# Performance work log

Hardware: AMD Instinct MI355X
Metric: run time of the kernel (lower is better)

The kernel has to match this reference:

```python
import jax, jax.numpy as jnp
import numpy as np

MIN_POS = 1e-6
EPS = 1e-20
B, S, F_IN, E, H = 2, 1024, 768, 768, 12
DH = E // H   # nnmf in_features per head (64)
FH = E // H   # nnmf out_features per head (hidden_features=embed_dim default)
N_NNMF_ITERS = 3
N_ALPHA_ITERS = 3


def l1norm(x, axis=-1):
    # F.normalize(x, p=1, dim=axis, eps=1e-20) for non-negative x
    return x / jnp.maximum(jnp.sum(jnp.abs(x), axis=axis, keepdims=True), EPS)


def setup_inputs() -> dict:
    key = jax.random.key(0)
    k = jax.random.split(key, 6)
    return {
        "x": jax.random.normal(k[0], (B, S, F_IN), jnp.float32),
        "embed_w": jax.random.normal(k[1], (E, F_IN), jnp.float32) * 0.02,
        "embed_b": jnp.zeros((E,), jnp.float32),
        "nnmf_w": jax.random.uniform(k[2], (FH, DH), jnp.float32),  # non-negative NMF dictionary
        "out_w": jax.random.normal(k[3], (F_IN, E), jnp.float32) * 0.02,
        "out_b": jnp.zeros((F_IN,), jnp.float32),
    }


def reference(x, embed_w, embed_b, nnmf_w, out_w, out_b):
    # normalize NMF weight rows (p=1 over in_features), as nnmf_layer.normalize_weights
    W = nnmf_w / jnp.maximum(jnp.sum(nnmf_w, axis=1, keepdims=True), EPS)  # [FH, DH]

    # embed + clamp positive, split heads
    xe = jnp.clip(x @ embed_w.T + embed_b, MIN_POS)            # [B,S,E]
    xe = xe.reshape(B, S, H, DH)                                # [B,S,H,DH]

    # NNMFDense: prepared_input = l1-normalized input (normalize_input_dim=-1)
    inp = l1norm(xe)                                            # [B,S,H,DH]
    h = l1norm(jnp.ones((B, S, H, FH), x.dtype))                # init hidden
    rec = inp
    for _ in range(N_NNMF_ITERS):
        rec = l1norm(jnp.clip(h @ W, MIN_POS))                  # reconstruction [B,S,H,DH]
        h = l1norm(jnp.clip(h * ((inp / rec) @ W.T), MIN_POS))  # multiplicative update

    # normalize_h (p=1, dim=-1)
    h = l1norm(h)                                               # [B,S,H,FH] -> 'bohf'

    # alpha dynamics fixed point
    alpha = jnp.ones((B, H, S, S), x.dtype)                     # 'bhoi'
    h_rec_input = rec * inp                                     # [B,S,H,DH]
    for _ in range(N_ALPHA_ITERS):
        h_mixed = jnp.einsum('bohf,bhoi->bihf', h, alpha)       # [B,S,H,FH]
        arec_inv = 1.0 / (h_mixed @ W + EPS)                    # _reconstruct -> [B,S,H,DH]
        alpha = alpha * jnp.einsum('bohf,bihf->bhoi', h_rec_input, arec_inv)

    out = jnp.einsum('bohf,bhoi->bihf', h, alpha)               # [B,S,H,FH]
    out = out.reshape(B, S, E)                                  # flatten heads
    return out @ out_w.T + out_b                                # out_project
```

## Files before the change

### kernel.cpp

```cpp
#include <hip/hip_runtime.h>

#define B_  2
#define S_  1024
#define FIN 768
#define E_  768
#define H_  12
#define DH  64

typedef unsigned int uint;
typedef unsigned short ushort;
typedef __attribute__((ext_vector_type(8))) short short8;
typedef __attribute__((ext_vector_type(4))) float floatx4;

__device__ __forceinline__ float bcast_lane(float v, int l) {
    return __uint_as_float((uint)__builtin_amdgcn_readlane((int)__float_as_uint(v), l));
}

__device__ __forceinline__ void wsum64x2(float& a, float& b) {
#pragma unroll
    for (int m = 1; m < 64; m <<= 1) {
        a += __shfl_xor(a, m, 64);
        b += __shfl_xor(b, m, 64);
    }
}

__device__ __forceinline__ ushort f2bf(float f) {
    uint u = __float_as_uint(f);
    return (ushort)((u + 0x7fffu + ((u >> 16) & 1u)) >> 16);
}

__device__ __forceinline__ uint4 pack8(const ushort* p) {
    uint4 r;
    r.x = (uint)p[0] | ((uint)p[1] << 16);
    r.y = (uint)p[2] | ((uint)p[3] << 16);
    r.z = (uint)p[4] | ((uint)p[5] << 16);
    r.w = (uint)p[6] | ((uint)p[7] << 16);
    return r;
}

__global__ __launch_bounds__(256) void k_wprep(const float* __restrict__ nw,
                                               float* __restrict__ Wn,
                                               float* __restrict__ WnT,
                                               float* __restrict__ r1inv,
                                               float* __restrict__ zbase) {
    const int tid = threadIdx.x;
    if (blockIdx.x == 0) {
        __shared__ float Wl[64 * 65];
        const int f = tid >> 2, q = tid & 3;
        float v[16];
        float s = 0.f;
#pragma unroll
        for (int i = 0; i < 16; ++i) { v[i] = nw[f * 64 + q * 16 + i]; s += v[i]; }
        s += __shfl_xor(s, 1, 64);
        s += __shfl_xor(s, 2, 64);
        const float inv = 1.f / fmaxf(s, 1e-20f);
#pragma unroll
        for (int i = 0; i < 16; ++i) {
            float w = v[i] * inv;
            Wn[f * 64 + q * 16 + i] = w;
            WnT[(q * 16 + i) * 64 + f] = w;
            Wl[f * 65 + q * 16 + i] = w;
        }
        __syncthreads();
        if (tid < 64) {
            float cs = 0.f;
            for (int ff = 0; ff < 64; ++ff) cs += Wl[ff * 65 + tid];
            float t = fmaxf(cs * (1.f / 64.f), 1e-6f);
            float S = t;
#pragma unroll
            for (int m = 1; m < 64; m <<= 1) S += __shfl_xor(S, m, 64);
            S = fmaxf(S, 1e-20f);
            r1inv[tid] = S / t;
        }
    } else {
        const int i = (blockIdx.x - 1) * 1024 + tid * 4;
        if (i < 26112) {
            float4 z = make_float4(0.f, 0.f, 0.f, 0.f);
            *(float4*)(zbase + i) = z;
        }
    }
}

__global__ __launch_bounds__(256) void k_embed(const float* __restrict__ xs,
                                               const float* __restrict__ ew,
                                               const float* __restrict__ eb,
                                               float* __restrict__ inp) {
    __shared__ ushort As_hi[64 * 72], As_lo[64 * 72];
    __shared__ ushort Bs_hi[64 * 72], Bs_lo[64 * 72];
    __shared__ float RS[2][64];
    const int tid = threadIdx.x;
    const int head = blockIdx.y;
    const int tok0 = blockIdx.x * 64;
    const int wv = tid >> 6, lane = tid & 63;
    const int mbase = (wv >> 1) * 32, nbase = (wv & 1) * 32;
    const int lm = lane & 15, lq = lane >> 4;

    floatx4 acc[2][2];
#pragma unroll
    for (int si = 0; si < 2; ++si)
#pragma unroll
        for (int ti = 0; ti < 2; ++ti) acc[si][ti] = (floatx4)0.f;

    const int row = tid >> 2;
    const int kq = (tid & 3) * 16;
    const float* xrow = xs + (size_t)(tok0 + row) * FIN + kq;
    const float* wrow = ew + (size_t)(head * 64 + row) * FIN + kq;

    float4 pa[4], pb[4];
#pragma unroll
    for (int c = 0; c < 4; ++c) {
        pa[c] = *(const float4*)(xrow + c * 4);
        pb[c] = *(const float4*)(wrow + c * 4);
    }

    for (int kb = 0; kb < FIN; kb += 64) {
        __syncthreads();
        {
            ushort ah[16], al[16], bh[16], bl[16];
#pragma unroll
            for (int c4 = 0; c4 < 4; ++c4) {
                float va[4] = {pa[c4].x, pa[c4].y, pa[c4].z, pa[c4].w};
                float vb[4] = {pb[c4].x, pb[c4].y, pb[c4].z, pb[c4].w};
#pragma unroll
                for (int j = 0; j < 4; ++j) {
                    ushort h = f2bf(va[j]);
                    ah[c4 * 4 + j] = h;
                    al[c4 * 4 + j] = f2bf(va[j] - __uint_as_float(((uint)h) << 16));
                    ushort g = f2bf(vb[j]);
                    bh[c4 * 4 + j] = g;
                    bl[c4 * 4 + j] = f2bf(vb[j] - __uint_as_float(((uint)g) << 16));
                }
            }
            const int off = row * 72 + kq;
            *(uint4*)&As_hi[off]     = pack8(ah);
            *(uint4*)&As_hi[off + 8] = pack8(ah + 8);
            *(uint4*)&As_lo[off]     = pack8(al);
            *(uint4*)&As_lo[off + 8] = pack8(al + 8);
            *(uint4*)&Bs_hi[off]     = pack8(bh);
            *(uint4*)&Bs_hi[off + 8] = pack8(bh + 8);
            *(uint4*)&Bs_lo[off]     = pack8(bl);
            *(uint4*)&Bs_lo[off + 8] = pack8(bl + 8);
        }
        __syncthreads();
        if (kb + 64 < FIN) {
#pragma unroll
            for (int c = 0; c < 4; ++c) {
                pa[c] = *(const float4*)(xrow + kb + 64 + c * 4);
                pb[c] = *(const float4*)(wrow + kb + 64 + c * 4);
            }
        }
#pragma unroll
        for (int ch = 0; ch < 2; ++ch) {
            const int ko = ch * 32 + lq * 8;
            short8 ah[2], al[2], bh[2], bl[2];
#pragma unroll
            for (int si = 0; si < 2; ++si) {
                ah[si] = *(const short8*)&As_hi[(mbase + si * 16 + lm) * 72 + ko];
                al[si] = *(const short8*)&As_lo[(mbase + si * 16 + lm) * 72 + ko];
            }
#pragma unroll
            for (int ti = 0; ti < 2; ++ti) {
                bh[ti] = *(const short8*)&Bs_hi[(nbase + ti * 16 + lm) * 72 + ko];
                bl[ti] = *(const short8*)&Bs_lo[(nbase + ti * 16 + lm) * 72 + ko];
            }
#pragma unroll
            for (int si = 0; si < 2; ++si)
#pragma unroll
                for (int ti = 0; ti < 2; ++ti) {
                    acc[si][ti] = __builtin_amdgcn_mfma_f32_16x16x32_bf16(
                        ah[si], bh[ti], acc[si][ti], 0, 0, 0);
                    acc[si][ti] = __builtin_amdgcn_mfma_f32_16x16x32_bf16(
                        al[si], bh[ti], acc[si][ti], 0, 0, 0);
                    acc[si][ti] = __builtin_amdgcn_mfma_f32_16x16x32_bf16(
                        ah[si], bl[ti], acc[si][ti], 0, 0, 0);
                }
        }
    }

    const int half = wv & 1;
    const float b0 = eb[head * 64 + nbase + lm];
    const float b1 = eb[head * 64 + nbase + 16 + lm];
    float xe[2][2][4];
#pragma unroll
    for (int si = 0; si < 2; ++si) {
        float rs[4];
#pragma unroll
        for (int r = 0; r < 4; ++r) {
            float e0 = fmaxf(acc[si][0][r] + b0, 1e-6f);
            float e1 = fmaxf(acc[si][1][r] + b1, 1e-6f);
            xe[si][0][r] = e0; xe[si][1][r] = e1;
            rs[r] = e0 + e1;
        }
#pragma unroll
        for (int r = 0; r < 4; ++r) {
            rs[r] += __shfl_xor(rs[r], 1, 64);
            rs[r] += __shfl_xor(rs[r], 2, 64);
            rs[r] += __shfl_xor(rs[r], 4, 64);
            rs[r] += __shfl_xor(rs[r], 8, 64);
        }
        if (lm == 0) {
#pragma unroll
            for (int r = 0; r < 4; ++r)
                RS[half][mbase + si * 16 + lq * 4 + r] = rs[r];
        }
    }
    __syncthreads();
    const size_t obase = ((size_t)((tok0 >> 10) * 12 + head) * 1024 + (tok0 & 1023));
#pragma unroll
    for (int si = 0; si < 2; ++si)
#pragma unroll
        for (int r = 0; r < 4; ++r) {
            const int m = mbase + si * 16 + lq * 4 + r;
            const float inv = 1.f / fmaxf(RS[0][m] + RS[1][m], 1e-20f);
            float* op = inp + (obase + m) * 64;
            op[nbase + lm]      = xe[si][0][r] * inv;
            op[nbase + 16 + lm] = xe[si][1][r] * inv;
        }
}

__global__ __launch_bounds__(256) void k_nnmf(const float* __restrict__ inp,
                                              const float* __restrict__ Wn,
                                              const float* __restrict__ WnT,
                                              const float* __restrict__ r1inv,
                                              float* __restrict__ hout,
                                              float* __restrict__ hriout,
                                              float* __restrict__ mp0) {
    const int tid = threadIdx.x;
    const int lane = tid & 63;
    float wcol[64], wrw[64];
#pragma unroll
    for (int f = 0; f < 64; ++f) wcol[f] = Wn[f * 64 + lane];
#pragma unroll
    for (int d = 0; d < 64; ++d) wrw[d] = WnT[d * 64 + lane];
    const float r1v = r1inv[lane];

    const int wid = blockIdx.x * 4 + (tid >> 6);
    float hsum = 0.f;
    for (int tt = 0; tt < 2; ++tt) {
        const int th0 = wid * 4 + tt * 2;
        const size_t base = (size_t)th0 * 64;
        float iv[2] = {inp[base + lane], inp[base + 64 + lane]};
        float hv[2], rec[2] = {0.f, 0.f};
        {
            float q[2] = {iv[0] * r1v, iv[1] * r1v};
            float ua[2] = {0.f, 0.f}, ub[2] = {0.f, 0.f};
#pragma unroll
            for (int d = 0; d < 64; d += 2) {
#pragma unroll
                for (int p = 0; p < 2; ++p) {
                    ua[p] = fmaf(bcast_lane(q[p], d    ), wrw[d    ], ua[p]);
                    ub[p] = fmaf(bcast_lane(q[p], d + 1), wrw[d + 1], ub[p]);
                }
            }
            float hn[2];
            hn[0] = fmaxf((ua[0] + ub[0]) * (1.f / 64.f), 1e-6f);
            hn[1] = fmaxf((ua[1] + ub[1]) * (1.f / 64.f), 1e-6f);
            float wn[2] = {hn[0], hn[1]};
            wsum64x2(wn[0], wn[1]);
            hv[0] = hn[0] / fmaxf(wn[0], 1e-20f);
            hv[1] = hn[1] / fmaxf(wn[1], 1e-20f);
        }
        for (int it = 0; it < 2; ++it) {
            float ta[2] = {0.f, 0.f}, tb[2] = {0.f, 0.f};
#pragma unroll
            for (int f = 0; f < 64; f += 2) {
#pragma unroll
                for (int p = 0; p < 2; ++p) {
                    ta[p] = fmaf(bcast_lane(hv[p], f    ), wcol[f    ], ta[p]);
                    tb[p] = fmaf(bcast_lane(hv[p], f + 1), wcol[f + 1], tb[p]);
                }
            }
            float t[2], w[2];
            t[0] = fmaxf(ta[0] + tb[0], 1e-6f);
            t[1] = fmaxf(ta[1] + tb[1], 1e-6f);
            w[0] = t[0]; w[1] = t[1];
            wsum64x2(w[0], w[1]);
            rec[0] = t[0] / fmaxf(w[0], 1e-20f);
            rec[1] = t[1] / fmaxf(w[1], 1e-20f);
            float q[2] = {iv[0] / rec[0], iv[1] / rec[1]};
            float ua[2] = {0.f, 0.f}, ub[2] = {0.f, 0.f};
#pragma unroll
            for (int d = 0; d < 64; d += 2) {
#pragma unroll
                for (int p = 0; p < 2; ++p) {
                    ua[p] = fmaf(bcast_lane(q[p], d    ), wrw[d    ], ua[p]);
                    ub[p] = fmaf(bcast_lane(q[p], d + 1), wrw[d + 1], ub[p]);
                }
            }
            float hn[2];
            hn[0] = fmaxf(hv[0] * (ua[0] + ub[0]), 1e-6f);
            hn[1] = fmaxf(hv[1] * (ua[1] + ub[1]), 1e-6f);
            float wn[2] = {hn[0], hn[1]};
            wsum64x2(wn[0], wn[1]);
            hv[0] = hn[0] / fmaxf(wn[0], 1e-20f);
            hv[1] = hn[1] / fmaxf(wn[1], 1e-20f);
        }
        float fs[2] = {hv[0], hv[1]};
        wsum64x2(fs[0], fs[1]);
        hv[0] = hv[0] / fmaxf(fs[0], 1e-20f);
        hv[1] = hv[1] / fmaxf(fs[1], 1e-20f);
        hout[base + lane] = hv[0];
        hout[base + 64 + lane] = hv[1];
        hriout[base + lane] = rec[0] * iv[0];
        hriout[base + 64 + lane] = rec[1] * iv[1];
        hsum += hv[0] + hv[1];
    }
    atomicAdd(&mp0[(size_t)(wid >> 4) * 64 + lane], hsum);
}

__global__ __launch_bounds__(256) void k_alpha_step(const float* __restrict__ hin,
                                                    const float* __restrict__ hri,
                                                    const float* __restrict__ Wn,
                                                    const float* __restrict__ mp_in,
                                                    float* __restrict__ mp_out,
                                                    float* __restrict__ c,
                                                    float* __restrict__ M,
                                                    int it) {
    __shared__ float mred[4][64];
    __shared__ float mv[64];
    __shared__ float vv[64];
    __shared__ float cl[64];
    const int tid = threadIdx.x;
    const int bh = blockIdx.x >> 4;
    const int chunk = blockIdx.x & 15;
    const size_t rowbase = (size_t)bh * 1024 + chunk * 64;

    {
        int f = tid & 63, p = tid >> 6;
        float s = 0.f;
#pragma unroll
        for (int pp = 0; pp < 4; ++pp)
            s += mp_in[((size_t)bh * 16 + p * 4 + pp) * 64 + f];
        mred[p][f] = s;
    }
    __syncthreads();
    if (tid < 64)
        mv[tid] = (mred[0][tid] + mred[1][tid]) + (mred[2][tid] + mred[3][tid]);
    __syncthreads();
    {
        int d = tid & 63, qq = tid >> 6;
        float r = 0.f;
#pragma unroll
        for (int ff = 0; ff < 16; ++ff)
            r = fmaf(mv[qq * 16 + ff], Wn[(size_t)(qq * 16 + ff) * 64 + d], r);
        mred[qq][d] = r;
    }
    __syncthreads();
    if (tid < 64)
        vv[tid] = 1.f / (((mred[0][tid] + mred[1][tid]) + (mred[2][tid] + mred[3][tid])) + 1e-20f);
    __syncthreads();
    {
        int o = tid >> 2, dq = tid & 3;
        const float* rp = hri + (rowbase + o) * 64 + dq * 16;
        float dot = 0.f;
#pragma unroll
        for (int t4 = 0; t4 < 16; t4 += 4) {
            float4 r4 = *(const float4*)(rp + t4);
            dot = fmaf(r4.x, vv[dq * 16 + t4 + 0], dot);
            dot = fmaf(r4.y, vv[dq * 16 + t4 + 1], dot);
            dot = fmaf(r4.z, vv[dq * 16 + t4 + 2], dot);
            dot = fmaf(r4.w, vv[dq * 16 + t4 + 3], dot);
        }
        dot += __shfl_xor(dot, 1, 64);
        dot += __shfl_xor(dot, 2, 64);
        float cn = dot;
        if (it >= 2) cn *= c[rowbase + o];
        if (dq == 0) { c[rowbase + o] = cn; cl[o] = cn; }
    }
    __syncthreads();
    {
        const int f4 = (tid & 15) * 4, ogr = tid >> 4;
        float4 a = make_float4(0.f, 0.f, 0.f, 0.f);
#pragma unroll
        for (int oi = 0; oi < 4; ++oi) {
            int o = ogr * 4 + oi;
            float4 h4 = *(const float4*)(hin + (rowbase + o) * 64 + f4);
            float cv = cl[o];
            a.x = fmaf(h4.x, cv, a.x); a.y = fmaf(h4.y, cv, a.y);
            a.z = fmaf(h4.z, cv, a.z); a.w = fmaf(h4.w, cv, a.w);
        }
        a.x += __shfl_xor(a.x, 16, 64); a.y += __shfl_xor(a.y, 16, 64);
        a.z += __shfl_xor(a.z, 16, 64); a.w += __shfl_xor(a.w, 16, 64);
        a.x += __shfl_xor(a.x, 32, 64); a.y += __shfl_xor(a.y, 32, 64);
        a.z += __shfl_xor(a.z, 32, 64); a.w += __shfl_xor(a.w, 32, 64);
        const int w = tid >> 6;
        if ((tid & 63) < 16) *(float4*)&mred[w][(tid & 15) * 4] = a;
    }
    __syncthreads();
    if (tid < 64) {
        float s = (mred[0][tid] + mred[1][tid]) + (mred[2][tid] + mred[3][tid]);
        if (it == 3) atomicAdd(&M[(size_t)bh * 64 + tid], s);
        else mp_out[((size_t)bh * 16 + chunk) * 64 + tid] = s;
    }
}

__global__ __launch_bounds__(256) void k_projbcast(const float* __restrict__ M,
                                                   const float* __restrict__ ow,
                                                   const float* __restrict__ ob,
                                                   float* __restrict__ out) {
    __shared__ float Ml[768];
    __shared__ float ps[4][64];
    __shared__ float yseg[64];
    const int tid = threadIdx.x;
    const int b = blockIdx.x / 192;
    const int rem = blockIdx.x - b * 192;
    const int jt = rem >> 4, rg = rem & 15;
    for (int i = tid; i < 768; i += 256) Ml[i] = M[b * 768 + i];
    __syncthreads();
    const int jj = tid & 63, part = tid >> 6;
    const int j = jt * 64 + jj;
    const float* row = ow + (size_t)j * 768 + part * 192;
    float acc = 0.f;
    for (int t = 0; t < 192; t += 4) {
        float4 w4 = *(const float4*)(row + t);
        acc = fmaf(w4.x, Ml[part * 192 + t + 0], acc);
        acc = fmaf(w4.y, Ml[part * 192 + t + 1], acc);
        acc = fmaf(w4.z, Ml[part * 192 + t + 2], acc);
        acc = fmaf(w4.w, Ml[part * 192 + t + 3], acc);
    }
    ps[part][jj] = acc;
    __syncthreads();
    if (tid < 64)
        yseg[tid] = ps[0][tid] + ps[1][tid] + ps[2][tid] + ps[3][tid] + ob[jt * 64 + tid];
    __syncthreads();
    const int r0 = tid >> 2, c4 = (tid & 3) * 16;
    float4 v4[4];
#pragma unroll
    for (int q = 0; q < 4; ++q) v4[q] = *(const float4*)&yseg[c4 + q * 4];
    float* dst = out + ((size_t)(b * 1024 + rg * 64 + r0)) * 768 + jt * 64 + c4;
#pragma unroll
    for (int q = 0; q < 4; ++q) *(float4*)(dst + q * 4) = v4[q];
}

extern "C" void kernel_launch(void* const* d_in, const int* in_sizes, int n_in,
                              void* d_out, int out_size, void* d_ws, size_t ws_size,
                              hipStream_t stream) {
    const float* xs = (const float*)d_in[0];
    const float* ew = (const float*)d_in[1];
    const float* eb = (const float*)d_in[2];
    const float* nw = (const float*)d_in[3];
    const float* ow = (const float*)d_in[4];
    const float* ob = (const float*)d_in[5];
    float* out = (float*)d_out;

    float* ws    = (float*)d_ws;
    float* inp   = ws;
    float* h     = ws + 1572864;
    float* hri   = ws + 3145728;
    float* Wn    = ws + 4718592;
    float* WnT   = ws + 4722688;
    float* r1inv = ws + 4726784;
    float* mp0   = ws + 4727040;
    float* M     = ws + 4751616;
    float* mp1   = ws + 4753152;
    float* mp2   = ws + 4777728;
    float* c     = ws + 4802304;

    k_wprep<<<27, 256, 0, stream>>>(nw, Wn, WnT, r1inv, mp0);
    k_embed<<<dim3(32, 12), 256, 0, stream>>>(xs, ew, eb, inp);
    k_nnmf<<<1536, 256, 0, stream>>>(inp, Wn, WnT, r1inv, h, hri, mp0);
    k_alpha_step<<<384, 256, 0, stream>>>(h, hri, Wn, mp0, mp1, c, M, 1);
    k_alpha_step<<<384, 256, 0, stream>>>(h, hri, Wn, mp1, mp2, c, M, 2);
    k_alpha_step<<<384, 256, 0, stream>>>(h, hri, Wn, mp2, mp1, c, M, 3);
    k_projbcast<<<384, 256, 0, stream>>>(M, ow, ob, out);
}
```

Measured before the change: 157.5 us.

## Rewrite NNMF iterations as bf16x3 MFMA matvecs over 16-row tiles

The per-token NNMF multiplicative updates move from scalar readlane-broadcast FMA loops to MFMA 16x16x32 bf16 products. Each operand is split into high and low bf16 parts and three products are summed to approximate fp32 accuracy. Each wave now processes 16 token-heads at a time, staging data through LDS to transpose the C layout into the A layout. Divisions become hardware reciprocals, and the grid shrinks to 384 blocks with per-block atomics into mp0. The risks are slightly lower precision, LDS round trips and barriers, and reduced occupancy.

After: 143.5 us. 1.1x faster.

```diff
diff --git a/kernel.cpp b/kernel.cpp
--- a/kernel.cpp
+++ b/kernel.cpp
@@ -11,18 +11,6 @@
 typedef unsigned short ushort;
 typedef __attribute__((ext_vector_type(8))) short short8;
 typedef __attribute__((ext_vector_type(4))) float floatx4;
-
-__device__ __forceinline__ float bcast_lane(float v, int l) {
-    return __uint_as_float((uint)__builtin_amdgcn_readlane((int)__float_as_uint(v), l));
-}
-
-__device__ __forceinline__ void wsum64x2(float& a, float& b) {
-#pragma unroll
-    for (int m = 1; m < 64; m <<= 1) {
-        a += __shfl_xor(a, m, 64);
-        b += __shfl_xor(b, m, 64);
-    }
-}
 
 __device__ __forceinline__ ushort f2bf(float f) {
     uint u = __float_as_uint(f);
@@ -36,6 +24,19 @@
     r.z = (uint)p[4] | ((uint)p[5] << 16);
     r.w = (uint)p[6] | ((uint)p[7] << 16);
     return r;
+}
+
+__device__ __forceinline__ void split8v(float4 a, float4 b, short8& hi, short8& lo) {
+    float v[8] = {a.x, a.y, a.z, a.w, b.x, b.y, b.z, b.w};
+    ushort h[8], l[8];
+#pragma unroll
+    for (int j = 0; j < 8; ++j) {
+        h[j] = f2bf(v[j]);
+        l[j] = f2bf(v[j] - __uint_as_float(((uint)h[j]) << 16));
+    }
+    uint4 H = pack8(h), L = pack8(l);
+    hi = *(short8*)&H;
+    lo = *(short8*)&L;
 }
 
 __global__ __launch_bounds__(256) void k_wprep(const float* __restrict__ nw,
@@ -218,6 +219,37 @@
         }
 }
 
+__device__ __forceinline__ void mfma_matvec(const float srcC[4][4], float* T,
+                                            int lm, int lq,
+                                            const short8 Bh[4][2],
+                                            const short8 Bl[4][2],
+                                            floatx4 out[4]) {
+#pragma unroll
+    for (int nt = 0; nt < 4; ++nt)
+#pragma unroll
+        for (int r = 0; r < 4; ++r)
+            T[(lq * 4 + r) * 68 + nt * 16 + lm] = srcC[nt][r];
+    __syncthreads();
+    float4 a00 = *(const float4*)&T[lm * 68 + lq * 8];
+    float4 a01 = *(const float4*)&T[lm * 68 + lq * 8 + 4];
+    float4 a10 = *(const float4*)&T[lm * 68 + 32 + lq * 8];
+    float4 a11 = *(const float4*)&T[lm * 68 + 32 + lq * 8 + 4];
+    short8 A0h, A0l, A1h, A1l;
+    split8v(a00, a01, A0h, A0l);
+    split8v(a10, a11, A1h, A1l);
+#pragma unroll
+    for (int nt = 0; nt < 4; ++nt) {
+        floatx4 acc = (floatx4)0.f;
+        acc = __builtin_amdgcn_mfma_f32_16x16x32_bf16(A0h, Bh[nt][0], acc, 0, 0, 0);
+        acc = __builtin_amdgcn_mfma_f32_16x16x32_bf16(A0l, Bh[nt][0], acc, 0, 0, 0);
+        acc = __builtin_amdgcn_mfma_f32_16x16x32_bf16(A0h, Bl[nt][0], acc, 0, 0, 0);
+        acc = __builtin_amdgcn_mfma_f32_16x16x32_bf16(A1h, Bh[nt][1], acc, 0, 0, 0);
+        acc = __builtin_amdgcn_mfma_f32_16x16x32_bf16(A1l, Bh[nt][1], acc, 0, 0, 0);
+        acc = __builtin_amdgcn_mfma_f32_16x16x32_bf16(A1h, Bl[nt][1], acc, 0, 0, 0);
+        out[nt] = acc;
+    }
+}
+
 __global__ __launch_bounds__(256) void k_nnmf(const float* __restrict__ inp,
                                               const float* __restrict__ Wn,
                                               const float* __restrict__ WnT,
@@ -225,87 +257,124 @@
                                               float* __restrict__ hout,
                                               float* __restrict__ hriout,
                                               float* __restrict__ mp0) {
-    const int tid = threadIdx.x;
-    const int lane = tid & 63;
-    float wcol[64], wrw[64];
-#pragma unroll
-    for (int f = 0; f < 64; ++f) wcol[f] = Wn[f * 64 + lane];
-#pragma unroll
-    for (int d = 0; d < 64; ++d) wrw[d] = WnT[d * 64 + lane];
-    const float r1v = r1inv[lane];
-
-    const int wid = blockIdx.x * 4 + (tid >> 6);
-    float hsum = 0.f;
-    for (int tt = 0; tt < 2; ++tt) {
-        const int th0 = wid * 4 + tt * 2;
-        const size_t base = (size_t)th0 * 64;
-        float iv[2] = {inp[base + lane], inp[base + 64 + lane]};
-        float hv[2], rec[2] = {0.f, 0.f};
-        {
-            float q[2] = {iv[0] * r1v, iv[1] * r1v};
-            float ua[2] = {0.f, 0.f}, ub[2] = {0.f, 0.f};
-#pragma unroll
-            for (int d = 0; d < 64; d += 2) {
-#pragma unroll
-                for (int p = 0; p < 2; ++p) {
-                    ua[p] = fmaf(bcast_lane(q[p], d    ), wrw[d    ], ua[p]);
-                    ub[p] = fmaf(bcast_lane(q[p], d + 1), wrw[d + 1], ub[p]);
-                }
+    __shared__ float Tb[4][16 * 68];
+    const int tid = threadIdx.x, wv = tid >> 6, lane = tid & 63;
+    const int lm = lane & 15, lq = lane >> 4;
+    float* T = Tb[wv];
+    const int rowbase = blockIdx.x * 64 + wv * 16;
+
+    short8 Bt_h[4][2], Bt_l[4][2], Bw_h[4][2], Bw_l[4][2];
+#pragma unroll
+    for (int nt = 0; nt < 4; ++nt)
+#pragma unroll
+        for (int kc = 0; kc < 2; ++kc) {
+            const int idx = (nt * 16 + lm) * 64 + kc * 32 + lq * 8;
+            split8v(*(const float4*)(WnT + idx), *(const float4*)(WnT + idx + 4),
+                    Bt_h[nt][kc], Bt_l[nt][kc]);
+            split8v(*(const float4*)(Wn + idx), *(const float4*)(Wn + idx + 4),
+                    Bw_h[nt][kc], Bw_l[nt][kc]);
+        }
+
+    float inpC[4][4];
+#pragma unroll
+    for (int nt = 0; nt < 4; ++nt)
+#pragma unroll
+        for (int r = 0; r < 4; ++r)
+            inpC[nt][r] = inp[(size_t)(rowbase + lq * 4 + r) * 64 + nt * 16 + lm];
+    float r1c[4];
+#pragma unroll
+    for (int nt = 0; nt < 4; ++nt) r1c[nt] = r1inv[nt * 16 + lm];
+
+    float hC[4][4], recC[4][4];
+    {
+        float qC[4][4];
+#pragma unroll
+        for (int nt = 0; nt < 4; ++nt)
+#pragma unroll
+            for (int r = 0; r < 4; ++r) qC[nt][r] = inpC[nt][r] * r1c[nt];
+        floatx4 u[4];
+        mfma_matvec(qC, T, lm, lq, Bw_h, Bw_l, u);
+#pragma unroll
+        for (int nt = 0; nt < 4; ++nt)
+#pragma unroll
+            for (int r = 0; r < 4; ++r)
+                hC[nt][r] = fmaxf(u[nt][r] * (1.f / 64.f), 1e-6f);
+#pragma unroll
+        for (int r = 0; r < 4; ++r) {
+            float s = (hC[0][r] + hC[1][r]) + (hC[2][r] + hC[3][r]);
+            s += __shfl_xor(s, 1, 64); s += __shfl_xor(s, 2, 64);
+            s += __shfl_xor(s, 4, 64); s += __shfl_xor(s, 8, 64);
+            const float inv = __builtin_amdgcn_rcpf(fmaxf(s, 1e-20f));
+#pragma unroll
+            for (int nt = 0; nt < 4; ++nt) hC[nt][r] *= inv;
+        }
+    }
+#pragma unroll 1
+    for (int it = 0; it < 2; ++it) {
+        floatx4 t[4];
+        mfma_matvec(hC, T, lm, lq, Bt_h, Bt_l, t);
+        float tC[4][4], qC[4][4];
+#pragma unroll
+        for (int nt = 0; nt < 4; ++nt)
+#pragma unroll
+            for (int r = 0; r < 4; ++r) tC[nt][r] = fmaxf(t[nt][r], 1e-6f);
+#pragma unroll
+        for (int r = 0; r < 4; ++r) {
+            float s = (tC[0][r] + tC[1][r]) + (tC[2][r] + tC[3][r]);
+            s += __shfl_xor(s, 1, 64); s += __shfl_xor(s, 2, 64);
+            s += __shfl_xor(s, 4, 64); s += __shfl_xor(s, 8, 64);
+            s = fmaxf(s, 1e-20f);
+            const float invS = __builtin_amdgcn_rcpf(s);
+#pragma unroll
+            for (int nt = 0; nt < 4; ++nt) {
+                recC[nt][r] = tC[nt][r] * invS;
+                qC[nt][r] = inpC[nt][r] * s * __builtin_amdgcn_rcpf(tC[nt][r]);
             }
-            float hn[2];
-            hn[0] = fmaxf((ua[0] + ub[0]) * (1.f / 64.f), 1e-6f);
-            hn[1] = fmaxf((ua[1] + ub[1]) * (1.f / 64.f), 1e-6f);
-            float wn[2] = {hn[0], hn[1]};
-            wsum64x2(wn[0], wn[1]);
-            hv[0] = hn[0] / fmaxf(wn[0], 1e-20f);
-            hv[1] = hn[1] / fmaxf(wn[1], 1e-20f);
-        }
-        for (int it = 0; it < 2; ++it) {
-            float ta[2] = {0.f, 0.f}, tb[2] = {0.f, 0.f};
-#pragma unroll
-            for (int f = 0; f < 64; f += 2) {
-#pragma unroll
-                for (int p = 0; p < 2; ++p) {
-                    ta[p] = fmaf(bcast_lane(hv[p], f    ), wcol[f    ], ta[p]);
-                    tb[p] = fmaf(bcast_lane(hv[p], f + 1), wcol[f + 1], tb[p]);
-                }
-            }
-            float t[2], w[2];
-            t[0] = fmaxf(ta[0] + tb[0], 1e-6f);
-            t[1] = fmaxf(ta[1] + tb[1], 1e-6f);
-            w[0] = t[0]; w[1] = t[1];
-            wsum64x2(w[0], w[1]);
-            rec[0] = t[0] / fmaxf(w[0], 1e-20f);
-            rec[1] = t[1] / fmaxf(w[1], 1e-20f);
-            float q[2] = {iv[0] / rec[0], iv[1] / rec[1]};
-            float ua[2] = {0.f, 0.f}, ub[2] = {0.f, 0.f};
-#pragma unroll
-            for (int d = 0; d < 64; d += 2) {
-#pragma unroll
-                for (int p = 0; p < 2; ++p) {
-                    ua[p] = fmaf(bcast_lane(q[p], d    ), wrw[d    ], ua[p]);
-                    ub[p] = fmaf(bcast_lane(q[p], d + 1), wrw[d + 1], ub[p]);
-                }
-            }
-            float hn[2];
-            hn[0] = fmaxf(hv[0] * (ua[0] + ub[0]), 1e-6f);
-            hn[1] = fmaxf(hv[1] * (ua[1] + ub[1]), 1e-6f);
-            float wn[2] = {hn[0], hn[1]};
-            wsum64x2(wn[0], wn[1]);
-            hv[0] = hn[0] / fmaxf(wn[0], 1e-20f);
-            hv[1] = hn[1] / fmaxf(wn[1], 1e-20f);
-        }
-        float fs[2] = {hv[0], hv[1]};
-        wsum64x2(fs[0], fs[1]);
-        hv[0] = hv[0] / fmaxf(fs[0], 1e-20f);
-        hv[1] = hv[1] / fmaxf(fs[1], 1e-20f);
-        hout[base + lane] = hv[0];
-        hout[base + 64 + lane] = hv[1];
-        hriout[base + lane] = rec[0] * iv[0];
-        hriout[base + 64 + lane] = rec[1] * iv[1];
-        hsum += hv[0] + hv[1];
-    }
-    atomicAdd(&mp0[(size_t)(wid >> 4) * 64 + lane], hsum);
+        }
+        floatx4 u[4];
+        mfma_matvec(qC, T, lm, lq, Bw_h, Bw_l, u);
+#pragma unroll
+        for (int nt = 0; nt < 4; ++nt)
+#pragma unroll
+            for (int r = 0; r < 4; ++r)
+                hC[nt][r] = fmaxf(hC[nt][r] * u[nt][r], 1e-6f);
+#pragma unroll
+        for (int r = 0; r < 4; ++r) {
+            float s = (hC[0][r] + hC[1][r]) + (hC[2][r] + hC[3][r]);
+            s += __shfl_xor(s, 1, 64); s += __shfl_xor(s, 2, 64);
+            s += __shfl_xor(s, 4, 64); s += __shfl_xor(s, 8, 64);
+            const float inv = __builtin_amdgcn_rcpf(fmaxf(s, 1e-20f));
+#pragma unroll
+            for (int nt = 0; nt < 4; ++nt) hC[nt][r] *= inv;
+        }
+    }
+#pragma unroll
+    for (int r = 0; r < 4; ++r) {
+        float s = (hC[0][r] + hC[1][r]) + (hC[2][r] + hC[3][r]);
+        s += __shfl_xor(s, 1, 64); s += __shfl_xor(s, 2, 64);
+        s += __shfl_xor(s, 4, 64); s += __shfl_xor(s, 8, 64);
+        const float inv = __builtin_amdgcn_rcpf(fmaxf(s, 1e-20f));
+#pragma unroll
+        for (int nt = 0; nt < 4; ++nt) hC[nt][r] *= inv;
+    }
+#pragma unroll
+    for (int nt = 0; nt < 4; ++nt)
+#pragma unroll
+        for (int r = 0; r < 4; ++r) {
+            const size_t o = (size_t)(rowbase + lq * 4 + r) * 64 + nt * 16 + lm;
+            hout[o] = hC[nt][r];
+            hriout[o] = recC[nt][r] * inpC[nt][r];
+        }
+    float hs[4];
+#pragma unroll
+    for (int nt = 0; nt < 4; ++nt) {
+        float s = (hC[nt][0] + hC[nt][1]) + (hC[nt][2] + hC[nt][3]);
+        s += __shfl_xor(s, 16, 64);
+        s += __shfl_xor(s, 32, 64);
+        hs[nt] = s;
+    }
+    float mvv = lq == 0 ? hs[0] : lq == 1 ? hs[1] : lq == 2 ? hs[2] : hs[3];
+    atomicAdd(&mp0[(size_t)blockIdx.x * 64 + lq * 16 + lm], mvv);
 }
 
 __global__ __launch_bounds__(256) void k_alpha_step(const float* __restrict__ hin,
@@ -458,7 +527,7 @@
 
     k_wprep<<<27, 256, 0, stream>>>(nw, Wn, WnT, r1inv, mp0);
     k_embed<<<dim3(32, 12), 256, 0, stream>>>(xs, ew, eb, inp);
-    k_nnmf<<<1536, 256, 0, stream>>>(inp, Wn, WnT, r1inv, h, hri, mp0);
+    k_nnmf<<<384, 256, 0, stream>>>(inp, Wn, WnT, r1inv, h, hri, mp0);
     k_alpha_step<<<384, 256, 0, stream>>>(h, hri, Wn, mp0, mp1, c, M, 1);
     k_alpha_step<<<384, 256, 0, stream>>>(h, hri, Wn, mp1, mp2, c, M, 2);
     k_alpha_step<<<384, 256, 0, stream>>>(h, hri, Wn, mp2, mp1, c, M, 3);
```
